# Kernel optimization log

Measured on AMD Instinct MI355X. Metric: run time of the kernel, lower is better.

Reference implementation:

```python
import jax, jax.numpy as jnp
import numpy as np

BETA = 1e10  # hard softmax temperature from the original module


def setup_inputs() -> dict:
    key = jax.random.key(0)
    ks = jax.random.split(key, 7)
    bs, nc, units, feat = 128, 1024, 512, 512
    return {
        "x": jax.random.normal(ks[0], (bs, feat), jnp.float32),
        "class_logits": jax.random.normal(ks[1], (bs, nc), jnp.float32),
        "h_states": jax.random.normal(ks[2], (nc, units), jnp.float32) * 0.1,
        "c_states": jax.random.normal(ks[3], (nc, units), jnp.float32) * 0.1,
        "kernel": jax.random.normal(ks[4], (feat, 4 * units), jnp.float32) * 0.05,
        "rec_kernel": jax.random.normal(ks[5], (units, 4 * units), jnp.float32) * 0.05,
        "bias": jnp.zeros((4 * units,), jnp.float32),
    }


def _diff_scatter(A, B, w):
    # A: (nc, u) old class states, B: (bs, u) new states, w: (bs, nc) hard softmax.
    # Faithful to tf version: broadcast to (nc, bs, u), blend, then reduce_max over bs.
    m = w.T[:, :, None]                       # (nc, bs, 1)
    blended = A[:, None, :] * (1.0 - m) + B[None, :, :] * m  # (nc, bs, u)
    return jnp.max(blended, axis=1)           # (nc, u)


def reference(x, class_logits, h_states, c_states, kernel, rec_kernel, bias):
    # diff_gather: softmax-weighted sum over classes == weights @ params
    w = jax.nn.softmax(class_logits * BETA, axis=-1)  # (bs, nc), ~one-hot
    h0 = w @ h_states                                  # (bs, u)
    c0 = w @ c_states                                  # (bs, u)

    # single-step Keras LSTM (seq_len == 1): gate order i, f, c, o
    z = x @ kernel + h0 @ rec_kernel + bias            # (bs, 4u)
    i, f, g, o = jnp.split(z, 4, axis=-1)
    i = jax.nn.sigmoid(i)
    f = jax.nn.sigmoid(f)
    g = jnp.tanh(g)
    o = jax.nn.sigmoid(o)
    c = f * c0 + i * g
    h = o * jnp.tanh(c)                                # LSTM output == h

    new_h = _diff_scatter(h_states, h, w)
    new_c = _diff_scatter(c_states, c, w)
    return h, new_h, new_c
```

## Files before the change

### kernel.cpp

```cpp
#include <hip/hip_runtime.h>
#include <hip/hip_bf16.h>
#include <math.h>

#define BS    128
#define NC    1024
#define UNITS 512
#define FEAT  512
#define FOURU 2048

typedef short bf16x8 __attribute__((ext_vector_type(8)));
typedef float f32x4  __attribute__((ext_vector_type(4)));

__device__ __forceinline__ short f2bf(float f) {
    union { float f; unsigned int u; } v; v.f = f;
    unsigned int r = (v.u + 0x7fffu + ((v.u >> 16) & 1u)) >> 16;
    return (short)r;
}

__global__ __launch_bounds__(256) void argmax_kernel(
    const float* __restrict__ logits, int* __restrict__ sidx)
{
    int b = blockIdx.x;
    int t = threadIdx.x;
    float best = -INFINITY; int bi = 0;
    for (int i = t; i < NC; i += 256) {
        float v = logits[b * NC + i];
        if (v > best) { best = v; bi = i; }
    }
    for (int off = 32; off > 0; off >>= 1) {
        float ov = __shfl_down(best, off);
        int   oi = __shfl_down(bi, off);
        if (ov > best || (ov == best && oi < bi)) { best = ov; bi = oi; }
    }
    __shared__ float sv[4]; __shared__ int si[4];
    int wid = t >> 6;
    if ((t & 63) == 0) { sv[wid] = best; si[wid] = bi; }
    __syncthreads();
    if (t == 0) {
        for (int w = 1; w < 4; ++w)
            if (sv[w] > best || (sv[w] == best && si[w] < bi)) { best = sv[w]; bi = si[w]; }
        sidx[b] = bi;
    }
}

#define NT   32
#define KC   32
#define APAD 40

__global__ __launch_bounds__(256) void gemm_kernel(
    const float* __restrict__ x, const float* __restrict__ h_states,
    const float* __restrict__ kern, const float* __restrict__ reck,
    const int* __restrict__ sidx, float* __restrict__ z)
{
    __shared__ __align__(16) short as[BS * APAD];
    __shared__ __align__(16) short wst[NT * APAD];
    __shared__ int sIdx[BS];

    int t = threadIdx.x;
    int ntile = blockIdx.x * NT;
    int kg = blockIdx.y;
    int kbase = kg * 256;
    bool useH = (kg >= 2);
    const float* W = useH ? reck : kern;
    int wkbase = useH ? (kbase - 512) : kbase;

    if (t < BS) sIdx[t] = sidx[t];
    __syncthreads();

    int wid = t >> 6, lane = t & 63;
    int l15 = lane & 15, quad = lane >> 4;

    f32x4 zero = {0.f, 0.f, 0.f, 0.f};
    f32x4 acc[2][2] = {{zero, zero}, {zero, zero}};

    for (int kstep = 0; kstep < 8; ++kstep) {
        int wk0 = wkbase + kstep * KC;

        {
            int k2 = (t & 15) * 2;
            int mb = t >> 4;
            for (int p = 0; p < 8; ++p) {
                int m = mb + p * 16;
                const float* src = useH ? (h_states + (long)sIdx[m] * UNITS + wk0 + k2)
                                        : (x + (long)m * FEAT + wk0 + k2);
                float2 v = *(const float2*)src;
                unsigned int pk = ((unsigned int)(unsigned short)f2bf(v.x)) |
                                  (((unsigned int)(unsigned short)f2bf(v.y)) << 16);
                *(unsigned int*)&as[m * APAD + k2] = pk;
            }
        }
        {
            int n  = t & 31;
            int kk0 = t >> 5;
            for (int p = 0; p < 4; ++p) {
                int kk = kk0 + p * 8;
                wst[n * APAD + kk] = f2bf(W[(long)(wk0 + kk) * FOURU + ntile + n]);
            }
        }
        __syncthreads();

        bf16x8 afrag[2], bfrag[2];
        for (int ms = 0; ms < 2; ++ms) {
            int m = wid * 32 + ms * 16 + l15;
            afrag[ms] = *(const bf16x8*)&as[m * APAD + quad * 8];
        }
        for (int ns = 0; ns < 2; ++ns) {
            int n = ns * 16 + l15;
            bfrag[ns] = *(const bf16x8*)&wst[n * APAD + quad * 8];
        }
        for (int ms = 0; ms < 2; ++ms)
            for (int ns = 0; ns < 2; ++ns)
                acc[ms][ns] = __builtin_amdgcn_mfma_f32_16x16x32_bf16(
                                  afrag[ms], bfrag[ns], acc[ms][ns], 0, 0, 0);
        __syncthreads();
    }

    for (int ms = 0; ms < 2; ++ms)
        for (int ns = 0; ns < 2; ++ns)
            for (int r = 0; r < 4; ++r) {
                int m = wid * 32 + ms * 16 + quad * 4 + r;
                int n = ntile + ns * 16 + l15;
                atomicAdd(&z[(long)m * FOURU + n], acc[ms][ns][r]);
            }
}

__global__ __launch_bounds__(256) void lstm_kernel(
    const float* __restrict__ z, const float* __restrict__ bias,
    const float* __restrict__ c_states, const int* __restrict__ sidx,
    float* __restrict__ h_out, float* __restrict__ c_buf)
{
    int e = blockIdx.x * 256 + threadIdx.x;
    int b = e >> 9;
    int u = e & 511;
    float zi = z[b * FOURU + u]          + bias[u];
    float zf = z[b * FOURU + 512 + u]    + bias[512 + u];
    float zg = z[b * FOURU + 1024 + u]   + bias[1024 + u];
    float zo = z[b * FOURU + 1536 + u]   + bias[1536 + u];
    float ig = 1.f / (1.f + expf(-zi));
    float fg = 1.f / (1.f + expf(-zf));
    float gg = tanhf(zg);
    float og = 1.f / (1.f + expf(-zo));
    float c0 = c_states[(long)sidx[b] * UNITS + u];
    float c  = fg * c0 + ig * gg;
    float h  = og * tanhf(c);
    h_out[e] = h;
    c_buf[e] = c;
}

__global__ __launch_bounds__(256) void scatter_kernel(
    const float* __restrict__ h_states, const float* __restrict__ c_states,
    const float* __restrict__ h_new, const float* __restrict__ c_new,
    const int* __restrict__ sidx,
    float* __restrict__ out_h, float* __restrict__ out_c)
{
    __shared__ int s[BS];
    int t = threadIdx.x;
    if (t < BS) s[t] = sidx[t];
    __syncthreads();
    int j = blockIdx.x >> 1;
    int u = (blockIdx.x & 1) * 256 + t;
    float mh = -INFINITY, mc = -INFINITY;
    int count = 0;
    for (int b = 0; b < BS; ++b) {
        if (s[b] == j) {
            ++count;
            mh = fmaxf(mh, h_new[b * UNITS + u]);
            mc = fmaxf(mc, c_new[b * UNITS + u]);
        }
    }
    float ah = h_states[(long)j * UNITS + u];
    float ac = c_states[(long)j * UNITS + u];
    out_h[(long)j * UNITS + u] = (count == BS) ? mh : fmaxf(ah, mh);
    out_c[(long)j * UNITS + u] = (count == BS) ? mc : fmaxf(ac, mc);
}

extern "C" void kernel_launch(void* const* d_in, const int* in_sizes, int n_in,
                              void* d_out, int out_size, void* d_ws, size_t ws_size,
                              hipStream_t stream)
{
    (void)in_sizes; (void)n_in; (void)out_size; (void)ws_size;
    const float* x      = (const float*)d_in[0];
    const float* logits = (const float*)d_in[1];
    const float* h_st   = (const float*)d_in[2];
    const float* c_st   = (const float*)d_in[3];
    const float* kern   = (const float*)d_in[4];
    const float* reck   = (const float*)d_in[5];
    const float* bias   = (const float*)d_in[6];

    float* out        = (float*)d_out;
    float* out_h_step = out;
    float* out_newh   = out + BS * UNITS;
    float* out_newc   = out + BS * UNITS + NC * UNITS;

    char*  ws   = (char*)d_ws;
    int*   sidx = (int*)ws;
    float* z    = (float*)(ws + 512);
    float* cbuf = (float*)(ws + 512 + BS * FOURU * sizeof(float));

    hipMemsetAsync(z, 0, BS * FOURU * sizeof(float), stream);
    argmax_kernel <<<BS, 256, 0, stream>>>(logits, sidx);
    gemm_kernel   <<<dim3(FOURU / NT, 4), 256, 0, stream>>>(x, h_st, kern, reck, sidx, z);
    lstm_kernel   <<<BS * UNITS / 256, 256, 0, stream>>>(z, bias, c_st, sidx, out_h_step, cbuf);
    scatter_kernel<<<NC * UNITS / 256, 256, 0, stream>>>(h_st, c_st, out_h_step, cbuf, sidx,
                                                         out_newh, out_newc);
}
```

Baseline: 116.3 us.

## Precompute bf16 A operand, split-K partial buffers, fuse LSTM into scatter

The argmax kernel now also gathers the selected h_states row and the x row, converting both to a packed bf16 matrix. The GEMM reads this matrix with a swizzled shared layout and writes split-K partials (8 K-groups) to separate buffers instead of using atomics, which drops the memset. The LSTM gate math is fused into the scatter kernel, which sums the partials per matching batch row and computes h and c on the fly. This removes two launches, the atomics, and the repeated per-tile conversion and gather of A. In exchange it adds an 8x partial-buffer read inside the scatter kernel and changes bf16 rounding to round-half-up.

```diff
diff --git a/kernel.cpp b/kernel.cpp
--- a/kernel.cpp
+++ b/kernel.cpp
@@ -7,18 +7,25 @@
 #define UNITS 512
 #define FEAT  512
 #define FOURU 2048
-
-typedef short bf16x8 __attribute__((ext_vector_type(8)));
-typedef float f32x4  __attribute__((ext_vector_type(4)));
-
-__device__ __forceinline__ short f2bf(float f) {
-    union { float f; unsigned int u; } v; v.f = f;
-    unsigned int r = (v.u + 0x7fffu + ((v.u >> 16) & 1u)) >> 16;
-    return (short)r;
-}
-
-__global__ __launch_bounds__(256) void argmax_kernel(
-    const float* __restrict__ logits, int* __restrict__ sidx)
+#define KG    8
+#define NT    32
+#define WPAD  40
+
+typedef short  bf16x8 __attribute__((ext_vector_type(8)));
+typedef float  f32x4  __attribute__((ext_vector_type(4)));
+
+__device__ __forceinline__ unsigned short bf_rhu(float f) {
+    union { float f; unsigned u; } v; v.f = f;
+    return (unsigned short)((v.u + 0x8000u) >> 16);
+}
+__device__ __forceinline__ unsigned pack2(float a, float b) {
+    return (unsigned)bf_rhu(a) | ((unsigned)bf_rhu(b) << 16);
+}
+
+__global__ __launch_bounds__(256) void argmax_prep_kernel(
+    const float* __restrict__ logits, const float* __restrict__ x,
+    const float* __restrict__ h_states,
+    int* __restrict__ sidx, unsigned* __restrict__ Abf )
 {
     int b = blockIdx.x;
     int t = threadIdx.x;
@@ -33,6 +40,7 @@
         if (ov > best || (ov == best && oi < bi)) { best = ov; bi = oi; }
     }
     __shared__ float sv[4]; __shared__ int si[4];
+    __shared__ int sbi;
     int wid = t >> 6;
     if ((t & 63) == 0) { sv[wid] = best; si[wid] = bi; }
     __syncthreads();
@@ -40,32 +48,32 @@
         for (int w = 1; w < 4; ++w)
             if (sv[w] > best || (sv[w] == best && si[w] < bi)) { best = sv[w]; bi = si[w]; }
         sidx[b] = bi;
-    }
-}
-
-#define NT   32
-#define KC   32
-#define APAD 40
+        sbi = bi;
+    }
+    __syncthreads();
+    int st = t & 127;
+    const float* srcrow = (t < 128) ? (x + (long)b * FEAT)
+                                    : (h_states + (long)sbi * UNITS);
+    float4 v = *(const float4*)(srcrow + st * 4);
+    unsigned lo = pack2(v.x, v.y), hi = pack2(v.z, v.w);
+    unsigned du = (unsigned)b * 512u + (t < 128 ? 0u : 256u) + (unsigned)st * 2u;
+    *(uint2*)(Abf + du) = make_uint2(lo, hi);
+}
 
 __global__ __launch_bounds__(256) void gemm_kernel(
-    const float* __restrict__ x, const float* __restrict__ h_states,
+    const unsigned short* __restrict__ Abf,
     const float* __restrict__ kern, const float* __restrict__ reck,
-    const int* __restrict__ sidx, float* __restrict__ z)
-{
-    __shared__ __align__(16) short as[BS * APAD];
-    __shared__ __align__(16) short wst[NT * APAD];
-    __shared__ int sIdx[BS];
+    float* __restrict__ z_part)
+{
+    __shared__ __align__(16) unsigned short as[BS * 32];
+    __shared__ __align__(16) unsigned short wst[NT * WPAD];
 
     int t = threadIdx.x;
     int ntile = blockIdx.x * NT;
     int kg = blockIdx.y;
-    int kbase = kg * 256;
-    bool useH = (kg >= 2);
-    const float* W = useH ? reck : kern;
-    int wkbase = useH ? (kbase - 512) : kbase;
-
-    if (t < BS) sIdx[t] = sidx[t];
-    __syncthreads();
+    const float* W = (kg < 4) ? kern : reck;
+    int wk0base = (kg & 3) * 128;
+    int k0base  = kg * 128;
 
     int wid = t >> 6, lane = t & 63;
     int l15 = lane & 15, quad = lane >> 4;
@@ -73,40 +81,33 @@
     f32x4 zero = {0.f, 0.f, 0.f, 0.f};
     f32x4 acc[2][2] = {{zero, zero}, {zero, zero}};
 
-    for (int kstep = 0; kstep < 8; ++kstep) {
-        int wk0 = wkbase + kstep * KC;
-
-        {
-            int k2 = (t & 15) * 2;
-            int mb = t >> 4;
-            for (int p = 0; p < 8; ++p) {
-                int m = mb + p * 16;
-                const float* src = useH ? (h_states + (long)sIdx[m] * UNITS + wk0 + k2)
-                                        : (x + (long)m * FEAT + wk0 + k2);
-                float2 v = *(const float2*)src;
-                unsigned int pk = ((unsigned int)(unsigned short)f2bf(v.x)) |
-                                  (((unsigned int)(unsigned short)f2bf(v.y)) << 16);
-                *(unsigned int*)&as[m * APAD + k2] = pk;
-            }
-        }
-        {
+    for (int kstep = 0; kstep < 4; ++kstep) {
+        int k0  = k0base  + kstep * 32;
+        int wk0 = wk0base + kstep * 32;
+
+        for (int r = 0; r < 2; ++r) {
+            int G = r * 256 + t;
+            int m = G >> 2;
+            int p = G & 3;
+            int c = (p ^ (m >> 1)) & 3;
+            bf16x8 v = *(const bf16x8*)(Abf + (long)m * 1024 + k0 + c * 8);
+            *(bf16x8*)&as[G * 8] = v;
+        }
+        for (int p = 0; p < 4; ++p) {
+            int kk = (t >> 5) + p * 8;
             int n  = t & 31;
-            int kk0 = t >> 5;
-            for (int p = 0; p < 4; ++p) {
-                int kk = kk0 + p * 8;
-                wst[n * APAD + kk] = f2bf(W[(long)(wk0 + kk) * FOURU + ntile + n]);
-            }
+            wst[n * WPAD + kk] = bf_rhu(W[(long)(wk0 + kk) * FOURU + ntile + n]);
         }
         __syncthreads();
 
         bf16x8 afrag[2], bfrag[2];
         for (int ms = 0; ms < 2; ++ms) {
             int m = wid * 32 + ms * 16 + l15;
-            afrag[ms] = *(const bf16x8*)&as[m * APAD + quad * 8];
+            afrag[ms] = *(const bf16x8*)&as[(m * 4 + ((quad ^ (m >> 1)) & 3)) * 8];
         }
         for (int ns = 0; ns < 2; ++ns) {
             int n = ns * 16 + l15;
-            bfrag[ns] = *(const bf16x8*)&wst[n * APAD + quad * 8];
+            bfrag[ns] = *(const bf16x8*)&wst[n * WPAD + quad * 8];
         }
         for (int ms = 0; ms < 2; ++ms)
             for (int ns = 0; ns < 2; ++ns)
@@ -115,43 +116,21 @@
         __syncthreads();
     }
 
+    float* zp = z_part + (long)kg * BS * FOURU;
     for (int ms = 0; ms < 2; ++ms)
         for (int ns = 0; ns < 2; ++ns)
             for (int r = 0; r < 4; ++r) {
                 int m = wid * 32 + ms * 16 + quad * 4 + r;
                 int n = ntile + ns * 16 + l15;
-                atomicAdd(&z[(long)m * FOURU + n], acc[ms][ns][r]);
+                zp[(long)m * FOURU + n] = acc[ms][ns][r];
             }
 }
 
-__global__ __launch_bounds__(256) void lstm_kernel(
-    const float* __restrict__ z, const float* __restrict__ bias,
-    const float* __restrict__ c_states, const int* __restrict__ sidx,
-    float* __restrict__ h_out, float* __restrict__ c_buf)
-{
-    int e = blockIdx.x * 256 + threadIdx.x;
-    int b = e >> 9;
-    int u = e & 511;
-    float zi = z[b * FOURU + u]          + bias[u];
-    float zf = z[b * FOURU + 512 + u]    + bias[512 + u];
-    float zg = z[b * FOURU + 1024 + u]   + bias[1024 + u];
-    float zo = z[b * FOURU + 1536 + u]   + bias[1536 + u];
-    float ig = 1.f / (1.f + expf(-zi));
-    float fg = 1.f / (1.f + expf(-zf));
-    float gg = tanhf(zg);
-    float og = 1.f / (1.f + expf(-zo));
-    float c0 = c_states[(long)sidx[b] * UNITS + u];
-    float c  = fg * c0 + ig * gg;
-    float h  = og * tanhf(c);
-    h_out[e] = h;
-    c_buf[e] = c;
-}
-
-__global__ __launch_bounds__(256) void scatter_kernel(
+__global__ __launch_bounds__(256) void scatter_lstm_kernel(
+    const float* __restrict__ z_part, const float* __restrict__ bias,
     const float* __restrict__ h_states, const float* __restrict__ c_states,
-    const float* __restrict__ h_new, const float* __restrict__ c_new,
     const int* __restrict__ sidx,
-    float* __restrict__ out_h, float* __restrict__ out_c)
+    float* __restrict__ h_out, float* __restrict__ out_h, float* __restrict__ out_c)
 {
     __shared__ int s[BS];
     int t = threadIdx.x;
@@ -159,17 +138,37 @@
     __syncthreads();
     int j = blockIdx.x >> 1;
     int u = (blockIdx.x & 1) * 256 + t;
+
+    float ah = h_states[(long)j * UNITS + u];
+    float ac = c_states[(long)j * UNITS + u];
+
     float mh = -INFINITY, mc = -INFINITY;
     int count = 0;
+    float bi_ = bias[u], bf_ = bias[512 + u], bg_ = bias[1024 + u], bo_ = bias[1536 + u];
+
     for (int b = 0; b < BS; ++b) {
         if (s[b] == j) {
             ++count;
-            mh = fmaxf(mh, h_new[b * UNITS + u]);
-            mc = fmaxf(mc, c_new[b * UNITS + u]);
-        }
-    }
-    float ah = h_states[(long)j * UNITS + u];
-    float ac = c_states[(long)j * UNITS + u];
+            float zi = bi_, zf = bf_, zg = bg_, zo = bo_;
+            #pragma unroll
+            for (int kg = 0; kg < KG; ++kg) {
+                const float* zp = z_part + (long)kg * BS * FOURU + (long)b * FOURU;
+                zi += zp[u];
+                zf += zp[512 + u];
+                zg += zp[1024 + u];
+                zo += zp[1536 + u];
+            }
+            float ig = 1.f / (1.f + expf(-zi));
+            float fg = 1.f / (1.f + expf(-zf));
+            float gg = tanhf(zg);
+            float og = 1.f / (1.f + expf(-zo));
+            float c  = fg * ac + ig * gg;
+            float h  = og * tanhf(c);
+            h_out[(long)b * UNITS + u] = h;
+            mh = fmaxf(mh, h);
+            mc = fmaxf(mc, c);
+        }
+    }
     out_h[(long)j * UNITS + u] = (count == BS) ? mh : fmaxf(ah, mh);
     out_c[(long)j * UNITS + u] = (count == BS) ? mc : fmaxf(ac, mc);
 }
@@ -192,15 +191,14 @@
     float* out_newh   = out + BS * UNITS;
     float* out_newc   = out + BS * UNITS + NC * UNITS;
 
-    char*  ws   = (char*)d_ws;
-    int*   sidx = (int*)ws;
-    float* z    = (float*)(ws + 512);
-    float* cbuf = (float*)(ws + 512 + BS * FOURU * sizeof(float));
-
-    hipMemsetAsync(z, 0, BS * FOURU * sizeof(float), stream);
-    argmax_kernel <<<BS, 256, 0, stream>>>(logits, sidx);
-    gemm_kernel   <<<dim3(FOURU / NT, 4), 256, 0, stream>>>(x, h_st, kern, reck, sidx, z);
-    lstm_kernel   <<<BS * UNITS / 256, 256, 0, stream>>>(z, bias, c_st, sidx, out_h_step, cbuf);
-    scatter_kernel<<<NC * UNITS / 256, 256, 0, stream>>>(h_st, c_st, out_h_step, cbuf, sidx,
-                                                         out_newh, out_newc);
-}
+    char*     ws     = (char*)d_ws;
+    int*      sidx   = (int*)ws;
+    unsigned* Abf    = (unsigned*)(ws + 1024);
+    float*    z_part = (float*)(ws + 1024 * 1024);
+
+    argmax_prep_kernel<<<BS, 256, 0, stream>>>(logits, x, h_st, sidx, Abf);
+    gemm_kernel<<<dim3(FOURU / NT, KG), 256, 0, stream>>>(
+        (const unsigned short*)Abf, kern, reck, z_part);
+    scatter_lstm_kernel<<<NC * UNITS / 256, 256, 0, stream>>>(
+        z_part, bias, h_st, c_st, sidx, out_h_step, out_newh, out_newc);
+}
```

Measured after the change: 105.8 us. -9.1%, faster.
